# Kernel tuning notes

Measured on AMD Instinct MI355X. Metric: run time of the kernel, lower is better.

## Reference

```python
import jax, jax.numpy as jnp
import numpy as np
from jax import lax

B, HS, WS_, DIM = 4, 64, 64, 512
NH, WSZ = 8, 2
WH, SH, HD = 4, 4, 64        # wavelet heads, window heads, head_dim
WDIM, SDIM, RED = 256, 256, 64  # w_dim, s_dim, w_dim//4
SCALE = HD ** -0.5
EPS = 1e-5


def dwt_haar(x):
    # x: [B,C,H,W] -> [B,4C,H/2,W/2]; exact haar 2x2 stride-2 depthwise conv
    a = x[:, :, 0::2, 0::2]; b = x[:, :, 0::2, 1::2]
    c = x[:, :, 1::2, 0::2]; d = x[:, :, 1::2, 1::2]
    ll = 0.5 * (a + b + c + d)
    lh = 0.5 * (a + b - c - d)
    hl = 0.5 * (a - b + c - d)
    hh = 0.5 * (a - b - c + d)
    return jnp.concatenate([ll, lh, hl, hh], axis=1)


def idwt_haar(x):
    # x: [B,4C,h,w] -> [B,C,2h,2w]; exact haar conv_transpose stride 2
    Bx, C4, h, w = x.shape
    C = C4 // 4
    ll, lh, hl, hh = jnp.split(x, 4, axis=1)
    y00 = 0.5 * (ll + lh + hl + hh)
    y01 = 0.5 * (ll + lh - hl - hh)
    y10 = 0.5 * (ll - lh + hl - hh)
    y11 = 0.5 * (ll - lh - hl + hh)
    top = jnp.stack([y00, y01], axis=-1).reshape(Bx, C, h, 2 * w)
    bot = jnp.stack([y10, y11], axis=-1).reshape(Bx, C, h, 2 * w)
    return jnp.stack([top, bot], axis=-2).reshape(Bx, C, 2 * h, 2 * w)


def bn2d(x, g, b):
    # eval-mode BatchNorm2d with running_mean=0, running_var=1
    s = g / jnp.sqrt(1.0 + EPS)
    return x * s[None, :, None, None] + b[None, :, None, None]


def layernorm(x, g, b):
    m = jnp.mean(x, axis=-1, keepdims=True)
    v = jnp.var(x, axis=-1, keepdims=True)
    return (x - m) / jnp.sqrt(v + EPS) * g + b


def wsda_forward(x, wq_w, kv_ln_g, kv_ln_b, wkv_w, wkv_b, wproj_w, wproj_b,
                 reduce_w, reduce_b, reduce_bn_g, reduce_bn_b,
                 filter_w, filter_b, filter_bn_g, filter_bn_b,
                 sqkv_w, sproj_w, sproj_b, H, W):
    Bx, N, C = x.shape
    x4 = x.reshape(Bx, H, W, C)  # ws divides H,W -> no padding

    # ---- windowed attention branch (sa) ----
    hg, wg = H // WSZ, W // WSZ
    G, L = hg * wg, WSZ * WSZ
    xg = x4.reshape(Bx, hg, WSZ, wg, WSZ, C).transpose(0, 1, 3, 2, 4, 5).reshape(Bx, G, L, C)
    qkv = (xg @ sqkv_w).reshape(Bx, G, L, 3, SH, HD)
    q = qkv[:, :, :, 0].transpose(0, 1, 3, 2, 4)  # [B,G,SH,L,HD]
    k = qkv[:, :, :, 1].transpose(0, 1, 3, 2, 4)
    v = qkv[:, :, :, 2].transpose(0, 1, 3, 2, 4)
    attn = jax.nn.softmax(jnp.einsum('bghld,bghmd->bghlm', q, k) * SCALE, axis=-1)
    o = jnp.einsum('bghlm,bghmd->bghld', attn, v)
    o = o.transpose(0, 1, 3, 2, 4).reshape(Bx, hg, wg, WSZ, WSZ, SDIM)
    o = o.transpose(0, 1, 3, 2, 4, 5).reshape(Bx, H, W, SDIM)
    sa_out = o @ sproj_w + sproj_b

    # ---- wavelet attention branch (wa) ----
    q = (x4.reshape(Bx, N, C) @ wq_w).reshape(Bx, N, WH, HD).transpose(0, 2, 1, 3)  # [B,WH,N,HD]
    xc = x4.transpose(0, 3, 1, 2)  # NCHW
    r = jnp.einsum('bchw,co->bohw', xc, reduce_w) + reduce_b[None, :, None, None]
    r = jax.nn.relu(bn2d(r, reduce_bn_g, reduce_bn_b))          # [B,RED,H,W]
    xd = dwt_haar(r)                                            # [B,WDIM,H/2,W/2]
    f = lax.conv_general_dilated(xd, filter_w, (1, 1), 'SAME',
                                 dimension_numbers=('NCHW', 'OIHW', 'NCHW'))
    f = f + filter_b[None, :, None, None]
    xd = jax.nn.relu(bn2d(f, filter_bn_g, filter_bn_b))         # [B,WDIM,H/2,W/2]
    xi = idwt_haar(xd)                                          # [B,RED,H,W]
    x_idwt = xi.reshape(Bx, RED, H * W).transpose(0, 2, 1)      # [B,N,RED]
    kv_in = xd.reshape(Bx, WDIM, -1).transpose(0, 2, 1)         # [B,M,WDIM], M=(H/2)(W/2)
    kv_in = layernorm(kv_in, kv_ln_g, kv_ln_b)
    kv = (kv_in @ wkv_w + wkv_b).reshape(Bx, -1, 2, WH, HD)
    kk = kv[:, :, 0].transpose(0, 2, 1, 3)                      # [B,WH,M,HD]
    vv = kv[:, :, 1].transpose(0, 2, 1, 3)
    attn = jax.nn.softmax(jnp.einsum('bhnd,bhmd->bhnm', q, kk) * SCALE, axis=-1)
    ow = jnp.einsum('bhnm,bhmd->bhnd', attn, vv).transpose(0, 2, 1, 3).reshape(Bx, N, WDIM)
    wa_out = (jnp.concatenate([ow, x_idwt], axis=-1) @ wproj_w + wproj_b).reshape(Bx, H, W, WDIM)

    out = jnp.concatenate([sa_out, wa_out], axis=-1).reshape(Bx, N, C)
    return out


def setup_inputs() -> dict:
    key = jax.random.key(0)
    ks = jax.random.split(key, 10)
    w = lambda k, s: jax.random.normal(k, s, jnp.float32) * 0.02
    return {
        'x': jax.random.normal(ks[0], (B, HS * WS_, DIM), jnp.float32),
        'wq_w': w(ks[1], (DIM, WDIM)),
        'kv_ln_g': jnp.ones((WDIM,), jnp.float32),
        'kv_ln_b': jnp.zeros((WDIM,), jnp.float32),
        'wkv_w': w(ks[2], (WDIM, 2 * WDIM)),
        'wkv_b': jnp.zeros((2 * WDIM,), jnp.float32),
        'wproj_w': w(ks[3], (WDIM + RED, WDIM)),
        'wproj_b': jnp.zeros((WDIM,), jnp.float32),
        'reduce_w': w(ks[4], (DIM, RED)),
        'reduce_b': jnp.zeros((RED,), jnp.float32),
        'reduce_bn_g': jnp.ones((RED,), jnp.float32),
        'reduce_bn_b': jnp.zeros((RED,), jnp.float32),
        'filter_w': w(ks[5], (WDIM, WDIM, 3, 3)),
        'filter_b': jnp.zeros((WDIM,), jnp.float32),
        'filter_bn_g': jnp.ones((WDIM,), jnp.float32),
        'filter_bn_b': jnp.zeros((WDIM,), jnp.float32),
        'sqkv_w': w(ks[6], (DIM, 3 * SDIM)),
        'sproj_w': w(ks[7], (SDIM, SDIM)),
        'sproj_b': jnp.zeros((SDIM,), jnp.float32),
        'H': HS,
        'W': WS_,
    }


def reference(x, wq_w, kv_ln_g, kv_ln_b, wkv_w, wkv_b, wproj_w, wproj_b,
              reduce_w, reduce_b, reduce_bn_g, reduce_bn_b,
              filter_w, filter_b, filter_bn_g, filter_bn_b,
              sqkv_w, sproj_w, sproj_b, H, W):
    return wsda_forward(x, wq_w, kv_ln_g, kv_ln_b, wkv_w, wkv_b, wproj_w, wproj_b,
                        reduce_w, reduce_b, reduce_bn_g, reduce_bn_b,
                        filter_w, filter_b, filter_bn_g, filter_bn_b,
                        sqkv_w, sproj_w, sproj_b, H, W)
```

## Files before the change

kernel.cpp:

```cpp
#include <hip/hip_runtime.h>
#include <hip/hip_bf16.h>
#include <math.h>

#define WEPS 1e-5f
#define WSCALE 0.125f
#define QSCALE 0.1803368801111244f

enum { EPI_NONE=0, EPI_BIAS=1, EPI_BN_RELU=2 };

typedef __attribute__((ext_vector_type(8))) short bf16x8;
typedef __attribute__((ext_vector_type(4))) float f32x4;

static __device__ inline unsigned short f2bf(float f) {
    __hip_bfloat16 h = __float2bfloat16(f);
    return *(unsigned short*)&h;
}
static __device__ inline float exp2_fast(float x) {
    float r;
    asm("v_exp_f32 %0, %1" : "=v"(r) : "v"(x));
    return r;
}
static __device__ inline unsigned cvt_pk_bf16(float a, float b) {
    unsigned r;
    asm("v_cvt_pk_bf16_f32 %0, %1, %2" : "=v"(r) : "v"(a), "v"(b));
    return r;
}
static __device__ inline void gload_lds16(const void* gsrc, void* ldst) {
    __builtin_amdgcn_global_load_lds(
        (const __attribute__((address_space(1))) unsigned int*)gsrc,
        (__attribute__((address_space(3))) unsigned int*)ldst, 16, 0, 0);
}
static __device__ inline int xcd_swizzle_id() {
    int id = blockIdx.x;
    int q = gridDim.x >> 3;
    return (id & 7) * q + (id >> 3);
}

static __device__ inline bf16x8 lds_frag(const unsigned short* base, int row, int inner) {
    int byte = row * 128 + (inner ^ ((row & 7) << 4));
    return *(const bf16x8*)((const char*)base + byte);
}
static __device__ inline bf16x8 lds_frag256(const unsigned short* base, int row, int inner) {
    int byte = row * 256 + (inner ^ ((row & 15) << 4));
    return *(const bf16x8*)((const char*)base + byte);
}

template<int EPI, int OBF16>
__launch_bounds__(256)
__global__ void gemm_bf16(const __hip_bfloat16* __restrict__ A, int lda,
                          const __hip_bfloat16* __restrict__ Bt, int K,
                          void* __restrict__ Cv, int ldc, int N, int nbx,
                          const float* __restrict__ bias,
                          const float* __restrict__ bn_g,
                          const float* __restrict__ bn_b,
                          float oscale)
{
    __shared__ unsigned short As[2][8192];
    __shared__ unsigned short Bs[2][8192];
    const int tid = threadIdx.x;
    const int lane = tid & 63, wv = tid >> 6;
    const int g = lane >> 4, l16 = lane & 15;
    const int wr = wv >> 1, wc = wv & 1;
    const int w = xcd_swizzle_id();
    const int bm = (w / nbx) << 7;
    const int bn = (w % nbx) << 7;

    int aoff[4], boff[4], ldst[4];
    #pragma unroll
    for (int it = 0; it < 4; it++) {
        int row = (it << 5) + (wv << 3) + (lane >> 3);
        int seg = (lane & 7) ^ (lane >> 3);
        aoff[it] = (bm + row) * lda + (seg << 3);
        boff[it] = (bn + row) * K + (seg << 3);
        ldst[it] = (it * 256 + tid) * 16;
    }
    f32x4 acc[4][4];
    #pragma unroll
    for (int i = 0; i < 4; i++)
        #pragma unroll
        for (int j = 0; j < 4; j++)
            #pragma unroll
            for (int r = 0; r < 4; r++) acc[i][j][r] = 0.f;

    #pragma unroll
    for (int it = 0; it < 4; it++) {
        gload_lds16(A + aoff[it], (char*)As[0] + ldst[it]);
        gload_lds16(Bt + boff[it], (char*)Bs[0] + ldst[it]);
    }
    __syncthreads();

    int cur = 0;
    const int niter = K >> 6;
    for (int t = 0; t < niter; t++) {
        if (t + 1 < niter) {
            int kb = (t + 1) << 6;
            #pragma unroll
            for (int it = 0; it < 4; it++) {
                gload_lds16(A + aoff[it] + kb, (char*)As[cur^1] + ldst[it]);
                gload_lds16(Bt + boff[it] + kb, (char*)Bs[cur^1] + ldst[it]);
            }
        }
        #pragma unroll
        for (int ks = 0; ks < 2; ks++) {
            bf16x8 af[4], bfr[4];
            #pragma unroll
            for (int i = 0; i < 4; i++)
                af[i] = lds_frag(As[cur], (wr<<6) + (i<<4) + l16, (ks<<6) + (g<<4));
            #pragma unroll
            for (int j = 0; j < 4; j++)
                bfr[j] = lds_frag(Bs[cur], (wc<<6) + (j<<4) + l16, (ks<<6) + (g<<4));
            #pragma unroll
            for (int i = 0; i < 4; i++)
                #pragma unroll
                for (int j = 0; j < 4; j++)
                    acc[i][j] = __builtin_amdgcn_mfma_f32_16x16x32_bf16(af[i], bfr[j], acc[i][j], 0, 0, 0);
        }
        __syncthreads();
        cur ^= 1;
    }
    const float bn_s = 0.99999500003749968f;
    #pragma unroll
    for (int i = 0; i < 4; i++) {
        int m = bm + (wr<<6) + (i<<4) + (g<<2);
        #pragma unroll
        for (int j = 0; j < 4; j++) {
            int c = bn + (wc<<6) + (j<<4) + l16;
            float bi = (EPI != EPI_NONE) ? bias[c] : 0.f;
            float sc = 1.f, bb = 0.f;
            if (EPI == EPI_BN_RELU) { sc = bn_g[c] * bn_s; bb = bn_b[c]; }
            #pragma unroll
            for (int r = 0; r < 4; r++) {
                float t = acc[i][j][r] * oscale + bi;
                if (EPI == EPI_BN_RELU) t = fmaxf(t * sc + bb, 0.f);
                if (OBF16) ((__hip_bfloat16*)Cv)[(size_t)(m+r)*ldc + c] = __float2bfloat16(t);
                else       ((float*)Cv)[(size_t)(m+r)*ldc + c] = t;
            }
        }
    }
}

__launch_bounds__(256)
__global__ void gemmX(const __hip_bfloat16* __restrict__ A,
                      const __hip_bfloat16* __restrict__ Bt,
                      __hip_bfloat16* __restrict__ qkvb,
                      __hip_bfloat16* __restrict__ qbw,
                      float* __restrict__ rbuf,
                      const float* __restrict__ red_b,
                      const float* __restrict__ rbn_g,
                      const float* __restrict__ rbn_b)
{
    __shared__ unsigned short As[2][8192];
    __shared__ unsigned short Bs[2][8192];
    const int tid = threadIdx.x;
    const int lane = tid & 63, wv = tid >> 6;
    const int g = lane >> 4, l16 = lane & 15;
    const int wr = wv >> 1, wc = wv & 1;
    const int w = xcd_swizzle_id();
    const int bm = (w / 9) << 7;
    const int bn = (w % 9) << 7;

    int aoff[4], boff[4], ldst[4];
    #pragma unroll
    for (int it = 0; it < 4; it++) {
        int row = (it << 5) + (wv << 3) + (lane >> 3);
        int seg = (lane & 7) ^ (lane >> 3);
        aoff[it] = (bm + row) * 512 + (seg << 3);
        boff[it] = (bn + row) * 512 + (seg << 3);
        ldst[it] = (it * 256 + tid) * 16;
    }
    f32x4 acc[4][4];
    #pragma unroll
    for (int i = 0; i < 4; i++)
        #pragma unroll
        for (int j = 0; j < 4; j++)
            #pragma unroll
            for (int r = 0; r < 4; r++) acc[i][j][r] = 0.f;

    #pragma unroll
    for (int it = 0; it < 4; it++) {
        gload_lds16(A + aoff[it], (char*)As[0] + ldst[it]);
        gload_lds16(Bt + boff[it], (char*)Bs[0] + ldst[it]);
    }
    __syncthreads();

    int cur = 0;
    for (int t = 0; t < 8; t++) {
        if (t < 7) {
            int kb = (t + 1) << 6;
            #pragma unroll
            for (int it = 0; it < 4; it++) {
                gload_lds16(A + aoff[it] + kb, (char*)As[cur^1] + ldst[it]);
                gload_lds16(Bt + boff[it] + kb, (char*)Bs[cur^1] + ldst[it]);
            }
        }
        #pragma unroll
        for (int ks = 0; ks < 2; ks++) {
            bf16x8 af[4], bfr[4];
            #pragma unroll
            for (int i = 0; i < 4; i++)
                af[i] = lds_frag(As[cur], (wr<<6) + (i<<4) + l16, (ks<<6) + (g<<4));
            #pragma unroll
            for (int j = 0; j < 4; j++)
                bfr[j] = lds_frag(Bs[cur], (wc<<6) + (j<<4) + l16, (ks<<6) + (g<<4));
            #pragma unroll
            for (int i = 0; i < 4; i++)
                #pragma unroll
                for (int j = 0; j < 4; j++)
                    acc[i][j] = __builtin_amdgcn_mfma_f32_16x16x32_bf16(af[i], bfr[j], acc[i][j], 0, 0, 0);
        }
        __syncthreads();
        cur ^= 1;
    }
    const float bn_s = 0.99999500003749968f;
    #pragma unroll
    for (int i = 0; i < 4; i++) {
        int m = bm + (wr<<6) + (i<<4) + (g<<2);
        #pragma unroll
        for (int j = 0; j < 4; j++) {
            int c = bn + (wc<<6) + (j<<4) + l16;
            if (c >= 1088) continue;
            if (c < 768) {
                #pragma unroll
                for (int r = 0; r < 4; r++)
                    qkvb[(size_t)(m+r)*768 + c] = __float2bfloat16(acc[i][j][r]);
            } else if (c < 1024) {
                int c2 = c - 768;
                #pragma unroll
                for (int r = 0; r < 4; r++)
                    qbw[(size_t)(m+r)*256 + c2] = __float2bfloat16(acc[i][j][r] * QSCALE);
            } else {
                int c2 = c - 1024;
                float sc = rbn_g[c2] * bn_s, bb = rbn_b[c2], bi = red_b[c2];
                #pragma unroll
                for (int r = 0; r < 4; r++)
                    rbuf[(size_t)(m+r)*64 + c2] = fmaxf((acc[i][j][r] + bi) * sc + bb, 0.f);
            }
        }
    }
}

__launch_bounds__(256)
__global__ void gemm64_kv(const __hip_bfloat16* __restrict__ A,
                          const __hip_bfloat16* __restrict__ Bt,
                          __hip_bfloat16* __restrict__ kbo,
                          __hip_bfloat16* __restrict__ vto,
                          const float* __restrict__ bias)
{
    __shared__ unsigned short As[2][4096];
    __shared__ unsigned short Bs[2][4096];
    const int tid = threadIdx.x;
    const int lane = tid & 63, wv = tid >> 6;
    const int g = lane >> 4, l16 = lane & 15;
    const int wr = wv >> 1, wc = wv & 1;
    const int bm = blockIdx.y << 6;
    const int bn = blockIdx.x << 6;

    int swb[2];
    const __hip_bfloat16 *Ap[2], *Bp[2];
    #pragma unroll
    for (int it = 0; it < 2; it++) {
        int idx = tid + (it << 8);
        int row = idx >> 3, seg = idx & 7;
        swb[it] = row * 128 + ((seg << 4) ^ ((row & 7) << 4));
        Ap[it] = A  + (size_t)(bm + row) * 256 + (seg << 3);
        Bp[it] = Bt + (size_t)(bn + row) * 256 + (seg << 3);
    }
    f32x4 acc[2][2];
    #pragma unroll
    for (int i = 0; i < 2; i++)
        #pragma unroll
        for (int j = 0; j < 2; j++)
            #pragma unroll
            for (int r = 0; r < 4; r++) acc[i][j][r] = 0.f;

    #pragma unroll
    for (int it = 0; it < 2; it++) {
        *(float4*)((char*)As[0] + swb[it]) = *(const float4*)(Ap[it]);
        *(float4*)((char*)Bs[0] + swb[it]) = *(const float4*)(Bp[it]);
    }
    __syncthreads();

    int cur = 0;
    for (int t = 0; t < 4; t++) {
        float4 ra[2], rb[2];
        const bool has_next = (t < 3);
        if (has_next) {
            #pragma unroll
            for (int it = 0; it < 2; it++) {
                ra[it] = *(const float4*)(Ap[it] + ((t + 1) << 6));
                rb[it] = *(const float4*)(Bp[it] + ((t + 1) << 6));
            }
        }
        #pragma unroll
        for (int ks = 0; ks < 2; ks++) {
            bf16x8 af[2], bfr[2];
            #pragma unroll
            for (int i = 0; i < 2; i++)
                af[i] = lds_frag(As[cur], (wr<<5) + (i<<4) + l16, (ks<<6) + (g<<4));
            #pragma unroll
            for (int j = 0; j < 2; j++)
                bfr[j] = lds_frag(Bs[cur], (wc<<5) + (j<<4) + l16, (ks<<6) + (g<<4));
            #pragma unroll
            for (int i = 0; i < 2; i++)
                #pragma unroll
                for (int j = 0; j < 2; j++)
                    acc[i][j] = __builtin_amdgcn_mfma_f32_16x16x32_bf16(af[i], bfr[j], acc[i][j], 0, 0, 0);
        }
        if (has_next) {
            #pragma unroll
            for (int it = 0; it < 2; it++) {
                *(float4*)((char*)As[cur^1] + swb[it]) = ra[it];
                *(float4*)((char*)Bs[cur^1] + swb[it]) = rb[it];
            }
        }
        __syncthreads();
        cur ^= 1;
    }

    #pragma unroll
    for (int i = 0; i < 2; i++) {
        int m = bm + (wr<<5) + (i<<4) + (g<<2);
        int bimg = m >> 10, tkn0 = m & 1023;
        #pragma unroll
        for (int j = 0; j < 2; j++) {
            int c = bn + (wc<<5) + (j<<4) + l16;
            if (c < 256) {
                int wh = c >> 6, d0 = c & 63;
                __hip_bfloat16* kp = kbo + (((size_t)((bimg<<2)+wh)) << 16) + (size_t)tkn0*64 + d0;
                #pragma unroll
                for (int r = 0; r < 4; r++)
                    kp[r*64] = __float2bfloat16(acc[i][j][r] + bias[c]);
            } else {
                int c2 = c - 256;
                int wh = c2 >> 6, d = c2 & 63;
                float bi = bias[256 + c2];
                ushort4 h;
                h.x = f2bf(acc[i][j][0] + bi);
                h.y = f2bf(acc[i][j][1] + bi);
                h.z = f2bf(acc[i][j][2] + bi);
                h.w = f2bf(acc[i][j][3] + bi);
                *(ushort4*)(vto + (((size_t)((bimg<<2)+wh)) << 16) + (size_t)d*1024 + tkn0) = h;
            }
        }
    }
}

__launch_bounds__(256)
__global__ void gemm_wproj(const __hip_bfloat16* __restrict__ A1,
                           const __hip_bfloat16* __restrict__ A2,
                           const __hip_bfloat16* __restrict__ Bt,
                           float* __restrict__ C,
                           const float* __restrict__ bias)
{
    __shared__ unsigned short As[2][8192];
    __shared__ unsigned short Bs[2][8192];
    const int tid = threadIdx.x;
    const int lane = tid & 63, wv = tid >> 6;
    const int g = lane >> 4, l16 = lane & 15;
    const int wr = wv >> 1, wc = wv & 1;
    const int w = xcd_swizzle_id();
    const int bm = (w >> 1) << 7;
    const int bn = (w & 1) << 7;

    int a1off[4], a2off[4], boff[4], ldst[4];
    #pragma unroll
    for (int it = 0; it < 4; it++) {
        int row = (it << 5) + (wv << 3) + (lane >> 3);
        int seg = (lane & 7) ^ (lane >> 3);
        a1off[it] = (bm + row) * 256 + (seg << 3);
        a2off[it] = (bm + row) * 64 + (seg << 3);
        boff[it]  = (bn + row) * 320 + (seg << 3);
        ldst[it]  = (it * 256 + tid) * 16;
    }
    f32x4 acc[4][4];
    #pragma unroll
    for (int i = 0; i < 4; i++)
        #pragma unroll
        for (int j = 0; j < 4; j++)
            #pragma unroll
            for (int r = 0; r < 4; r++) acc[i][j][r] = 0.f;

    #pragma unroll
    for (int it = 0; it < 4; it++) {
        gload_lds16(A1 + a1off[it], (char*)As[0] + ldst[it]);
        gload_lds16(Bt + boff[it], (char*)Bs[0] + ldst[it]);
    }
    __syncthreads();

    int cur = 0;
    for (int t = 0; t < 5; t++) {
        if (t < 4) {
            int kb = (t + 1) << 6;
            #pragma unroll
            for (int it = 0; it < 4; it++) {
                if (kb < 256)
                    gload_lds16(A1 + a1off[it] + kb, (char*)As[cur^1] + ldst[it]);
                else
                    gload_lds16(A2 + a2off[it], (char*)As[cur^1] + ldst[it]);
                gload_lds16(Bt + boff[it] + kb, (char*)Bs[cur^1] + ldst[it]);
            }
        }
        #pragma unroll
        for (int ks = 0; ks < 2; ks++) {
            bf16x8 af[4], bfr[4];
            #pragma unroll
            for (int i = 0; i < 4; i++)
                af[i] = lds_frag(As[cur], (wr<<6) + (i<<4) + l16, (ks<<6) + (g<<4));
            #pragma unroll
            for (int j = 0; j < 4; j++)
                bfr[j] = lds_frag(Bs[cur], (wc<<6) + (j<<4) + l16, (ks<<6) + (g<<4));
            #pragma unroll
            for (int i = 0; i < 4; i++)
                #pragma unroll
                for (int j = 0; j < 4; j++)
                    acc[i][j] = __builtin_amdgcn_mfma_f32_16x16x32_bf16(af[i], bfr[j], acc[i][j], 0, 0, 0);
        }
        __syncthreads();
        cur ^= 1;
    }
    #pragma unroll
    for (int i = 0; i < 4; i++) {
        int m = bm + (wr<<6) + (i<<4) + (g<<2);
        #pragma unroll
        for (int j = 0; j < 4; j++) {
            int c = bn + (wc<<6) + (j<<4) + l16;
            float bi = bias[c];
            #pragma unroll
            for (int r = 0; r < 4; r++)
                C[(size_t)(m+r)*512 + c] = acc[i][j][r] + bi;
        }
    }
}

__launch_bounds__(256)
__global__ void conv3_mfma(const __hip_bfloat16* __restrict__ Xd,
                           const __hip_bfloat16* __restrict__ Wt,
                           float* __restrict__ C,
                           const float* __restrict__ bias,
                           const float* __restrict__ bn_g,
                           const float* __restrict__ bn_b)
{
    __shared__ unsigned short As[2][8192];
    __shared__ unsigned short Bs[2][8192];
    const int tid = threadIdx.x;
    const int lane = tid & 63, wv = tid >> 6;
    const int g = lane >> 4, l16 = lane & 15;
    const int wr = wv >> 1, wc = wv & 1;
    const int bm = blockIdx.y << 6;
    const int bn = blockIdx.x << 6;

    int srow[4], sseg[4], swb[4];
    #pragma unroll
    for (int it = 0; it < 4; it++) {
        int idx = tid + (it << 8);
        srow[it] = idx >> 4;
        sseg[it] = idx & 15;
        swb[it]  = srow[it] * 256 + ((sseg[it] << 4) ^ ((srow[it] & 15) << 4));
    }
    int abase[4], ay[4], ax[4];
    #pragma unroll
    for (int it = 0; it < 4; it++) {
        int m = bm + srow[it];
        int bimg = m >> 10, s = m & 1023;
        ay[it] = s >> 5; ax[it] = s & 31;
        abase[it] = bimg << 10;
    }

    f32x4 acc[2][2];
    #pragma unroll
    for (int i = 0; i < 2; i++)
        #pragma unroll
        for (int j = 0; j < 2; j++)
            #pragma unroll
            for (int r = 0; r < 4; r++) acc[i][j][r] = 0.f;

    #pragma unroll
    for (int it = 0; it < 4; it++) {
        int y = ay[it] - 1, xx = ax[it] - 1;
        float4 av = make_float4(0.f,0.f,0.f,0.f);
        if ((unsigned)y < 32u && (unsigned)xx < 32u)
            av = *(const float4*)(Xd + ((size_t)(abase[it] + (y<<5) + xx) << 8) + (sseg[it] << 3));
        *(float4*)((char*)As[0] + swb[it]) = av;
        float4 bv = *(const float4*)(Wt + (size_t)(bn + srow[it]) * 2304 + (sseg[it] << 3));
        *(float4*)((char*)Bs[0] + swb[it]) = bv;
    }
    __syncthreads();

    int cur = 0;
    for (int t = 0; t < 18; t++) {
        float4 ra[4], rb[4];
        const bool has_next = (t + 1 < 18);
        if (has_next) {
            int tn = t + 1;
            int tap = tn >> 1;
            int dy = tap / 3 - 1;
            int dx = tap - (tap / 3) * 3 - 1;
            int i0 = (tn & 1) << 7;
            #pragma unroll
            for (int it = 0; it < 4; it++) {
                int y = ay[it] + dy, xx = ax[it] + dx;
                ra[it] = make_float4(0.f,0.f,0.f,0.f);
                if ((unsigned)y < 32u && (unsigned)xx < 32u)
                    ra[it] = *(const float4*)(Xd + ((size_t)(abase[it] + (y<<5) + xx) << 8) + i0 + (sseg[it] << 3));
                rb[it] = *(const float4*)(Wt + (size_t)(bn + srow[it]) * 2304 + tn * 128 + (sseg[it] << 3));
            }
        }
        #pragma unroll
        for (int ks = 0; ks < 4; ks++) {
            bf16x8 af[2], bfr[2];
            #pragma unroll
            for (int i = 0; i < 2; i++)
                af[i] = lds_frag256(As[cur], (wr<<5) + (i<<4) + l16, (ks<<6) + (g<<4));
            #pragma unroll
            for (int j = 0; j < 2; j++)
                bfr[j] = lds_frag256(Bs[cur], (wc<<5) + (j<<4) + l16, (ks<<6) + (g<<4));
            #pragma unroll
            for (int i = 0; i < 2; i++)
                #pragma unroll
                for (int j = 0; j < 2; j++)
                    acc[i][j] = __builtin_amdgcn_mfma_f32_16x16x32_bf16(af[i], bfr[j], acc[i][j], 0, 0, 0);
        }
        if (has_next) {
            #pragma unroll
            for (int it = 0; it < 4; it++) {
                *(float4*)((char*)As[cur^1] + swb[it]) = ra[it];
                *(float4*)((char*)Bs[cur^1] + swb[it]) = rb[it];
            }
        }
        __syncthreads();
        cur ^= 1;
    }

    const float bn_s = 0.99999500003749968f;
    #pragma unroll
    for (int i = 0; i < 2; i++) {
        int m = bm + (wr<<5) + (i<<4) + (g<<2);
        #pragma unroll
        for (int j = 0; j < 2; j++) {
            int c = bn + (wc<<5) + (j<<4) + l16;
            float sc = bn_g[c] * bn_s, bb = bn_b[c], bi = bias[c];
            #pragma unroll
            for (int r = 0; r < 4; r++)
                C[(size_t)(m + r) * 256 + c] = fmaxf((acc[i][j][r] + bi) * sc + bb, 0.f);
        }
    }
}

static __device__ inline void tr_task(const float* in, __hip_bfloat16* o,
                                      int K, int N, int nb, int tid)
{
    int idx = nb * 256 + tid;
    int n = idx / K, k = idx - n * K;
    o[idx] = __float2bfloat16(in[(size_t)k * N + n]);
}

__global__ void prep_all(const float* __restrict__ x,
                         const float* __restrict__ sqkv_w, const float* __restrict__ wq_w,
                         const float* __restrict__ reduce_w, const float* __restrict__ sproj_w,
                         const float* __restrict__ wkv_w, const float* __restrict__ wproj_w,
                         const float* __restrict__ filter_w,
                         __hip_bfloat16* __restrict__ xb, __hip_bfloat16* __restrict__ sqkvT,
                         __hip_bfloat16* __restrict__ wqT, __hip_bfloat16* __restrict__ redT,
                         __hip_bfloat16* __restrict__ sprojT, __hip_bfloat16* __restrict__ wkvT,
                         __hip_bfloat16* __restrict__ wprojT, __hip_bfloat16* __restrict__ wt2b)
{
    int bid = blockIdx.x, tid = threadIdx.x;
    if (bid < 8192) {
        int i = bid * 256 + tid;
        float4 v = ((const float4*)x)[i];
        ushort4 h;
        h.x = f2bf(v.x); h.y = f2bf(v.y); h.z = f2bf(v.z); h.w = f2bf(v.w);
        *(ushort4*)(xb + (size_t)i * 4) = h;
        return;
    }
    bid -= 8192;
    if (bid < 1536) { tr_task(sqkv_w, sqkvT, 512, 768, bid, tid); return; }
    bid -= 1536;
    if (bid < 512)  { tr_task(wq_w, wqT, 512, 256, bid, tid); return; }
    bid -= 512;
    if (bid < 128)  { tr_task(reduce_w, redT, 512, 64, bid, tid); return; }
    bid -= 128;
    if (bid < 256)  { tr_task(sproj_w, sprojT, 256, 256, bid, tid); return; }
    bid -= 256;
    if (bid < 512)  { tr_task(wkv_w, wkvT, 256, 512, bid, tid); return; }
    bid -= 512;
    if (bid < 320)  { tr_task(wproj_w, wprojT, 320, 256, bid, tid); return; }
    bid -= 320;
    {
        int oc = bid;
        const float* src = filter_w + (size_t)(oc * 256 + tid) * 9;
        __hip_bfloat16* dst = wt2b + (size_t)oc * 2304 + tid;
        #pragma unroll
        for (int tap = 0; tap < 9; tap++)
            dst[tap * 256] = __float2bfloat16(src[tap]);
    }
}

__launch_bounds__(256)
__global__ void win_attn(const __hip_bfloat16* __restrict__ qkv,
                         __hip_bfloat16* __restrict__ sa_o)
{
    int gw = blockIdx.x * 4 + (threadIdx.x >> 6);
    int lane = threadIdx.x & 63;
    int b  = gw >> 12;
    int g  = (gw >> 2) & 1023;
    int sh = gw & 3;
    int hg = g >> 5, wg = g & 31;
    float q[4], k[4], v[4];
    int rows[4];
    #pragma unroll
    for (int l = 0; l < 4; l++) {
        int h = (hg << 1) + (l >> 1), w = (wg << 1) + (l & 1);
        int row = (b << 12) + (h << 6) + w;
        rows[l] = row;
        const __hip_bfloat16* p = qkv + (size_t)row * 768 + sh * 64 + lane;
        q[l] = __bfloat162float(p[0]);
        k[l] = __bfloat162float(p[256]);
        v[l] = __bfloat162float(p[512]);
    }
    float s[4][4];
    #pragma unroll
    for (int l = 0; l < 4; l++)
        #pragma unroll
        for (int m = 0; m < 4; m++) s[l][m] = q[l] * k[m];
    #pragma unroll
    for (int off = 32; off > 0; off >>= 1)
        #pragma unroll
        for (int l = 0; l < 4; l++)
            #pragma unroll
            for (int m = 0; m < 4; m++)
                s[l][m] += __shfl_xor(s[l][m], off, 64);
    #pragma unroll
    for (int l = 0; l < 4; l++) {
        float s0 = s[l][0]*WSCALE, s1 = s[l][1]*WSCALE, s2 = s[l][2]*WSCALE, s3 = s[l][3]*WSCALE;
        float mx = fmaxf(fmaxf(s0,s1), fmaxf(s2,s3));
        float p0 = __expf(s0-mx), p1 = __expf(s1-mx), p2 = __expf(s2-mx), p3 = __expf(s3-mx);
        float inv = 1.f / (p0+p1+p2+p3);
        float o = (p0*v[0] + p1*v[1] + p2*v[2] + p3*v[3]) * inv;
        sa_o[(size_t)rows[l] * 256 + sh * 64 + lane] = __float2bfloat16(o);
    }
}

__global__ void dwt_kernel(const float* __restrict__ r, __hip_bfloat16* __restrict__ xd)
{
    int t = blockIdx.x * 256 + threadIdx.x;
    int o = t & 63;
    int x = (t >> 6) & 31;
    int y = (t >> 11) & 31;
    int b = t >> 16;
    const float* rb = r + (b << 18);
    int base = ((y << 1) << 6) + (x << 1);
    float a  = rb[(base     ) * 64 + o];
    float bb = rb[(base +  1) * 64 + o];
    float c  = rb[(base + 64) * 64 + o];
    float d  = rb[(base + 65) * 64 + o];
    float ll = 0.5f*(a+bb+c+d), lh = 0.5f*(a+bb-c-d);
    float hl = 0.5f*(a-bb+c-d), hh = 0.5f*(a-bb-c+d);
    __hip_bfloat16* outp = xd + (((b << 10) + (y << 5) + x) << 8) + o;
    outp[0]   = __float2bfloat16(ll);
    outp[64]  = __float2bfloat16(lh);
    outp[128] = __float2bfloat16(hl);
    outp[192] = __float2bfloat16(hh);
}

__launch_bounds__(256)
__global__ void ln_idwt(const float* __restrict__ X, const float* __restrict__ g,
                        const float* __restrict__ bta, __hip_bfloat16* __restrict__ Y,
                        __hip_bfloat16* __restrict__ xi)
{
    int bid = blockIdx.x;
    int t = threadIdx.x;
    if (bid < 4096) {
        int row = bid;
        float x = X[(size_t)row * 256 + t];
        __shared__ float red[4];
        int wv = t >> 6, ln = t & 63;
        float s = x;
        #pragma unroll
        for (int off = 32; off > 0; off >>= 1) s += __shfl_xor(s, off, 64);
        if (ln == 0) red[wv] = s;
        __syncthreads();
        float m = (red[0]+red[1]+red[2]+red[3]) * (1.f/256.f);
        float d = x - m;
        float s2 = d * d;
        #pragma unroll
        for (int off = 32; off > 0; off >>= 1) s2 += __shfl_xor(s2, off, 64);
        __syncthreads();
        if (ln == 0) red[wv] = s2;
        __syncthreads();
        float var = (red[0]+red[1]+red[2]+red[3]) * (1.f/256.f);
        float inv = 1.f / sqrtf(var + WEPS);
        Y[(size_t)row * 256 + t] = __float2bfloat16(d * inv * g[t] + bta[t]);
        return;
    }
    int tt = (bid - 4096) * 256 + t;
    int o = tt & 63;
    int x = (tt >> 6) & 31;
    int y = (tt >> 11) & 31;
    int b = tt >> 16;
    const float* p = X + (((b << 10) + (y << 5) + x) << 8);
    float ll = p[o], lh = p[64+o], hl = p[128+o], hh = p[192+o];
    float y00 = 0.5f*(ll+lh+hl+hh);
    float y01 = 0.5f*(ll+lh-hl-hh);
    float y10 = 0.5f*(ll-lh+hl-hh);
    float y11 = 0.5f*(ll-lh-hl+hh);
    __hip_bfloat16* ob = xi + ((size_t)b << 18);
    int base = ((y << 1) << 6) + (x << 1);
    ob[(size_t)(base     ) * 64 + o] = __float2bfloat16(y00);
    ob[(size_t)(base +  1) * 64 + o] = __float2bfloat16(y01);
    ob[(size_t)(base + 64) * 64 + o] = __float2bfloat16(y10);
    ob[(size_t)(base + 65) * 64 + o] = __float2bfloat16(y11);
}

__launch_bounds__(256)
__global__ void flash_mfma(const __hip_bfloat16* __restrict__ qb,
                           const __hip_bfloat16* __restrict__ kb,
                           const __hip_bfloat16* __restrict__ vt,
                           __hip_bfloat16* __restrict__ ow)
{
    __shared__ unsigned short Ks[4096];
    __shared__ unsigned short Vs[4096];
    const int tid = threadIdx.x;
    const int wv = tid >> 6;
    const int lane = tid & 63;
    const int g = lane >> 4, q16 = lane & 15;
    const int bh = blockIdx.y;
    const int b = bh >> 2, wh = bh & 3;
    const int qbase = (blockIdx.x << 6) + (wv << 4);

    const __hip_bfloat16* qp = qb + ((size_t)((b << 12) + qbase + q16)) * 256 + wh * 64 + g * 8;
    bf16x8 qf0 = *(const bf16x8*)qp;
    bf16x8 qf1 = *(const bf16x8*)(qp + 32);

    const __hip_bfloat16* kbase = kb + ((size_t)bh << 16);
    const __hip_bfloat16* vbase = vt + ((size_t)bh << 16);

    f32x4 oacc[4];
    #pragma unroll
    for (int dc = 0; dc < 4; dc++)
        #pragma unroll
        for (int r = 0; r < 4; r++) oacc[dc][r] = 0.f;
    float m_cur = -1e30f;
    float lsum_part = 0.f;

    for (int t0 = 0; t0 < 1024; t0 += 64) {
        __syncthreads();
        #pragma unroll
        for (int it = 0; it < 2; it++) {
            int off = (tid << 4) + (it << 12);
            int row = off >> 7;
            int inner = off & 127;
            int wb = row * 128 + (inner ^ ((row & 7) << 4));
            float4 kd = *(const float4*)(kbase + (t0 + row) * 64 + (inner >> 1));
            float4 vd = *(const float4*)(vbase + row * 1024 + t0 + (inner >> 1));
            *(float4*)((char*)Ks + wb) = kd;
            *(float4*)((char*)Vs + wb) = vd;
        }
        __syncthreads();

        f32x4 st[4];
        __builtin_amdgcn_s_setprio(1);
        #pragma unroll
        for (int sub = 0; sub < 4; sub++) {
            #pragma unroll
            for (int r = 0; r < 4; r++) st[sub][r] = 0.f;
            bf16x8 k0 = lds_frag(Ks, sub * 16 + q16, g * 16);
            bf16x8 k1 = lds_frag(Ks, sub * 16 + q16, 64 + g * 16);
            st[sub] = __builtin_amdgcn_mfma_f32_16x16x32_bf16(k0, qf0, st[sub], 0, 0, 0);
            st[sub] = __builtin_amdgcn_mfma_f32_16x16x32_bf16(k1, qf1, st[sub], 0, 0, 0);
        }
        __builtin_amdgcn_s_setprio(0);

        float pmax = -1e30f;
        #pragma unroll
        for (int t = 0; t < 4; t++)
            #pragma unroll
            for (int r = 0; r < 4; r++) pmax = fmaxf(pmax, st[t][r]);
        if (!__all(pmax <= m_cur + 11.5f)) {
            float mx = pmax;
            mx = fmaxf(mx, __shfl_xor(mx, 16, 64));
            mx = fmaxf(mx, __shfl_xor(mx, 32, 64));
            float m_new = fmaxf(m_cur, mx);
            float alpha = exp2_fast(m_cur - m_new);
            lsum_part *= alpha;
            #pragma unroll
            for (int r = 0; r < 4; r++) {
                float sc = __shfl(alpha, (g << 2) + r, 64);
                #pragma unroll
                for (int dc = 0; dc < 4; dc++) oacc[dc][r] *= sc;
            }
            m_cur = m_new;
        }

        float psum = 0.f;
        unsigned pk[4][2];
        #pragma unroll
        for (int t = 0; t < 4; t++) {
            float p0 = exp2_fast(st[t][0] - m_cur), p1 = exp2_fast(st[t][1] - m_cur);
            float p2 = exp2_fast(st[t][2] - m_cur), p3 = exp2_fast(st[t][3] - m_cur);
            psum += (p0 + p1) + (p2 + p3);
            pk[t][0] = cvt_pk_bf16(p0, p1);
            pk[t][1] = cvt_pk_bf16(p2, p3);
        }
        lsum_part += psum;

        bool ghi = (g & 2) != 0;
        unsigned pkA0[2], pkA1[2];
        pkA0[0] = ghi ? pk[1][0] : pk[0][0];
        pkA0[1] = ghi ? pk[1][1] : pk[0][1];
        pkA1[0] = ghi ? pk[3][0] : pk[2][0];
        pkA1[1] = ghi ? pk[3][1] : pk[2][1];
        union { int u[4]; bf16x8 v; } A0, A1;
        #pragma unroll
        for (int c = 0; c < 4; c++) {
            int src = (((2 * g + (c >> 1)) & 3) << 4) | q16;
            A0.u[c] = __shfl((int)pkA0[c & 1], src, 64);
            A1.u[c] = __shfl((int)pkA1[c & 1], src, 64);
        }

        __builtin_amdgcn_s_setprio(1);
        #pragma unroll
        for (int dc = 0; dc < 4; dc++) {
            bf16x8 v0 = lds_frag(Vs, dc * 16 + q16, g * 16);
            bf16x8 v1 = lds_frag(Vs, dc * 16 + q16, 64 + g * 16);
            oacc[dc] = __builtin_amdgcn_mfma_f32_16x16x32_bf16(A0.v, v0, oacc[dc], 0, 0, 0);
            oacc[dc] = __builtin_amdgcn_mfma_f32_16x16x32_bf16(A1.v, v1, oacc[dc], 0, 0, 0);
        }
        __builtin_amdgcn_s_setprio(0);
    }

    lsum_part += __shfl_xor(lsum_part, 16, 64);
    lsum_part += __shfl_xor(lsum_part, 32, 64);
    #pragma unroll
    for (int r = 0; r < 4; r++) {
        float inv = 1.f / __shfl(lsum_part, (g << 2) + r, 64);
        int qrow = (b << 12) + qbase + (g << 2) + r;
        #pragma unroll
        for (int dc = 0; dc < 4; dc++)
            ow[(size_t)qrow * 256 + wh * 64 + dc * 16 + q16] =
                __float2bfloat16(oacc[dc][r] * inv);
    }
}

extern "C" void kernel_launch(void* const* d_in, const int* in_sizes, int n_in,
                              void* d_out, int out_size, void* d_ws, size_t ws_size,
                              hipStream_t stream)
{
    const float* x        = (const float*)d_in[0];
    const float* wq_w     = (const float*)d_in[1];
    const float* kv_ln_g  = (const float*)d_in[2];
    const float* kv_ln_b  = (const float*)d_in[3];
    const float* wkv_w    = (const float*)d_in[4];
    const float* wkv_b    = (const float*)d_in[5];
    const float* wproj_w  = (const float*)d_in[6];
    const float* wproj_b  = (const float*)d_in[7];
    const float* reduce_w = (const float*)d_in[8];
    const float* reduce_b = (const float*)d_in[9];
    const float* rbn_g    = (const float*)d_in[10];
    const float* rbn_b    = (const float*)d_in[11];
    const float* filter_w = (const float*)d_in[12];
    const float* filter_b = (const float*)d_in[13];
    const float* fbn_g    = (const float*)d_in[14];
    const float* fbn_b    = (const float*)d_in[15];
    const float* sqkv_w   = (const float*)d_in[16];
    const float* sproj_w  = (const float*)d_in[17];
    const float* sproj_b  = (const float*)d_in[18];
    float* out = (float*)d_out;
    float* ws  = (float*)d_ws;

    __hip_bfloat16* qkvb  = (__hip_bfloat16*)(ws);
    __hip_bfloat16* owb   = (__hip_bfloat16*)(ws);
    __hip_bfloat16* sa_ob = (__hip_bfloat16*)(ws + 6291456);
    __hip_bfloat16* xb    = (__hip_bfloat16*)(ws + 8388608);
    __hip_bfloat16* sqkvT = (__hip_bfloat16*)(ws + 12582912);
    __hip_bfloat16* wqT   = (__hip_bfloat16*)(ws + 12779520);
    __hip_bfloat16* redT  = (__hip_bfloat16*)(ws + 12845056);
    __hip_bfloat16* sprojT= (__hip_bfloat16*)(ws + 12861440);
    __hip_bfloat16* wkvT  = (__hip_bfloat16*)(ws + 12894208);
    __hip_bfloat16* wprojT= (__hip_bfloat16*)(ws + 13025280);
    __hip_bfloat16* wt2b  = (__hip_bfloat16*)(ws + 13066240);
    float* rbuf  = ws + 13361152;
    __hip_bfloat16* xd1b  = (__hip_bfloat16*)(ws + 14409728);
    float* xd2   = ws + 14934016;
    __hip_bfloat16* kvinb = (__hip_bfloat16*)(ws + 15982592);
    __hip_bfloat16* xidwtb= (__hip_bfloat16*)(ws + 16506880);
    __hip_bfloat16* qbw   = (__hip_bfloat16*)(ws + 17031168);
    __hip_bfloat16* kbb   = (__hip_bfloat16*)(ws + 19128320);
    __hip_bfloat16* vtb   = (__hip_bfloat16*)(ws + 19652608);

    dim3 blk(256);

    prep_all<<<dim3(11712), blk, 0, stream>>>(x, sqkv_w, wq_w, reduce_w, sproj_w,
                                              wkv_w, wproj_w, filter_w,
                                              xb, sqkvT, wqT, redT, sprojT, wkvT,
                                              wprojT, wt2b);

    gemmX<<<dim3(1152), blk, 0, stream>>>(xb, sqkvT, qkvb, qbw, rbuf,
                                          reduce_b, rbn_g, rbn_b);
    win_attn<<<dim3(4096), blk, 0, stream>>>(qkvb, sa_ob);
    gemm_bf16<EPI_BIAS,0><<<dim3(256), blk, 0, stream>>>(sa_ob, 256, sprojT, 256, out, 512,
                                                         256, 2, sproj_b, nullptr, nullptr, 1.f);
    dwt_kernel<<<dim3(1024), blk, 0, stream>>>(rbuf, xd1b);
    conv3_mfma<<<dim3(4,64), blk, 0, stream>>>(xd1b, wt2b, xd2, filter_b, fbn_g, fbn_b);
    ln_idwt<<<dim3(5120), blk, 0, stream>>>(xd2, kv_ln_g, kv_ln_b, kvinb, xidwtb);
    gemm64_kv<<<dim3(8,64), blk, 0, stream>>>(kvinb, wkvT, kbb, vtb, wkv_b);
    flash_mfma<<<dim3(64,16), blk, 0, stream>>>(qbw, kbb, vtb, owb);
    gemm_wproj<<<dim3(256), blk, 0, stream>>>(owb, xidwtb, wprojT, out + 256, wproj_b);
}
```

Before: 147.8 us.

## Double-buffer K/V tiles in flash attention with direct global-to-LDS loads

The flash attention kernel now keeps two LDS buffers for K and V and prefetches the next 64-key tile with direct global-to-LDS loads while the current tile is computed. This replaces the register-staged load plus two barriers per iteration with one barrier at the end of each iteration, so memory latency can overlap with MFMA work. LDS use doubles to 32KB per block, which may reduce occupancy. Correctness relies on gload_lds16 completing before the barrier, i.e. on the helper's vmcnt waits.

```diff
diff --git a/kernel.cpp b/kernel.cpp
--- a/kernel.cpp
+++ b/kernel.cpp
@@ -718,8 +718,8 @@
                            const __hip_bfloat16* __restrict__ vt,
                            __hip_bfloat16* __restrict__ ow)
 {
-    __shared__ unsigned short Ks[4096];
-    __shared__ unsigned short Vs[4096];
+    __shared__ unsigned short Ks[2][4096];
+    __shared__ unsigned short Vs[2][4096];
     const int tid = threadIdx.x;
     const int wv = tid >> 6;
     const int lane = tid & 63;
@@ -735,6 +735,17 @@
     const __hip_bfloat16* kbase = kb + ((size_t)bh << 16);
     const __hip_bfloat16* vbase = vt + ((size_t)bh << 16);
 
+    int koff[2], voff[2], ldst[2];
+    #pragma unroll
+    for (int it = 0; it < 2; it++) {
+        int slot = tid + (it << 8);
+        int row = slot >> 3;
+        int seg = (slot & 7) ^ (row & 7);
+        koff[it] = row * 64 + (seg << 3);
+        voff[it] = row * 1024 + (seg << 3);
+        ldst[it] = slot * 16;
+    }
+
     f32x4 oacc[4];
     #pragma unroll
     for (int dc = 0; dc < 4; dc++)
@@ -743,20 +754,22 @@
     float m_cur = -1e30f;
     float lsum_part = 0.f;
 
+    #pragma unroll
+    for (int it = 0; it < 2; it++) {
+        gload_lds16(kbase + koff[it], (char*)Ks[0] + ldst[it]);
+        gload_lds16(vbase + voff[it], (char*)Vs[0] + ldst[it]);
+    }
+    __syncthreads();
+
+    int cur = 0;
     for (int t0 = 0; t0 < 1024; t0 += 64) {
-        __syncthreads();
-        #pragma unroll
-        for (int it = 0; it < 2; it++) {
-            int off = (tid << 4) + (it << 12);
-            int row = off >> 7;
-            int inner = off & 127;
-            int wb = row * 128 + (inner ^ ((row & 7) << 4));
-            float4 kd = *(const float4*)(kbase + (t0 + row) * 64 + (inner >> 1));
-            float4 vd = *(const float4*)(vbase + row * 1024 + t0 + (inner >> 1));
-            *(float4*)((char*)Ks + wb) = kd;
-            *(float4*)((char*)Vs + wb) = vd;
-        }
-        __syncthreads();
+        if (t0 + 64 < 1024) {
+            #pragma unroll
+            for (int it = 0; it < 2; it++) {
+                gload_lds16(kbase + koff[it] + (t0 + 64) * 64, (char*)Ks[cur^1] + ldst[it]);
+                gload_lds16(vbase + voff[it] + (t0 + 64), (char*)Vs[cur^1] + ldst[it]);
+            }
+        }
 
         f32x4 st[4];
         __builtin_amdgcn_s_setprio(1);
@@ -764,8 +777,8 @@
         for (int sub = 0; sub < 4; sub++) {
             #pragma unroll
             for (int r = 0; r < 4; r++) st[sub][r] = 0.f;
-            bf16x8 k0 = lds_frag(Ks, sub * 16 + q16, g * 16);
-            bf16x8 k1 = lds_frag(Ks, sub * 16 + q16, 64 + g * 16);
+            bf16x8 k0 = lds_frag(Ks[cur], sub * 16 + q16, g * 16);
+            bf16x8 k1 = lds_frag(Ks[cur], sub * 16 + q16, 64 + g * 16);
             st[sub] = __builtin_amdgcn_mfma_f32_16x16x32_bf16(k0, qf0, st[sub], 0, 0, 0);
             st[sub] = __builtin_amdgcn_mfma_f32_16x16x32_bf16(k1, qf1, st[sub], 0, 0, 0);
         }
@@ -821,12 +834,15 @@
         __builtin_amdgcn_s_setprio(1);
         #pragma unroll
         for (int dc = 0; dc < 4; dc++) {
-            bf16x8 v0 = lds_frag(Vs, dc * 16 + q16, g * 16);
-            bf16x8 v1 = lds_frag(Vs, dc * 16 + q16, 64 + g * 16);
+            bf16x8 v0 = lds_frag(Vs[cur], dc * 16 + q16, g * 16);
+            bf16x8 v1 = lds_frag(Vs[cur], dc * 16 + q16, 64 + g * 16);
             oacc[dc] = __builtin_amdgcn_mfma_f32_16x16x32_bf16(A0.v, v0, oacc[dc], 0, 0, 0);
             oacc[dc] = __builtin_amdgcn_mfma_f32_16x16x32_bf16(A1.v, v1, oacc[dc], 0, 0, 0);
         }
         __builtin_amdgcn_s_setprio(0);
+
+        __syncthreads();
+        cur ^= 1;
     }
 
     lsum_part += __shfl_xor(lsum_part, 16, 64);
```

Measured after the change: 149.4 us. Within noise of the previous version (+1.1%).
